# Kernel tuning notes

Measured on AMD Instinct MI355X. Metric: run time of the kernel, lower is better.

## Reference

```python
import jax, jax.numpy as jnp
import numpy as np

NUM_Q = 1000
DIM_S = 64
SIZE_M = 50
BATCH = 128
SEQ = 200


def setup_inputs() -> dict:
    key = jax.random.key(0)
    ks = jax.random.split(key, 16)
    s = 1.0 / np.sqrt(DIM_S)
    inp = {
        "q": jax.random.randint(ks[0], (BATCH, SEQ), 0, NUM_Q),
        "r": jax.random.randint(ks[1], (BATCH, SEQ), 0, 2),
        "at_s": jax.random.randint(ks[2], (BATCH, 16), 0, 30000),
        "at_m": jnp.ones((BATCH, 16), dtype=jnp.int64 if jax.config.jax_enable_x64 else jnp.int32),
        "k_emb": jax.random.normal(ks[3], (NUM_Q, DIM_S)) * s,
        "v_emb": jax.random.normal(ks[4], (2 * NUM_Q, DIM_S)) * s,
        "Mk": jax.random.normal(ks[5], (SIZE_M, DIM_S)) * s,
        "Mv0": jax.random.normal(ks[6], (SIZE_M, DIM_S)) * s,
        "We": jax.random.normal(ks[7], (DIM_S, DIM_S)) * s,
        "be": jnp.zeros((DIM_S,)),
        "Wa": jax.random.normal(ks[8], (DIM_S, DIM_S)) * s,
        "ba": jnp.zeros((DIM_S,)),
        "Wf": jax.random.normal(ks[9], (2 * DIM_S, DIM_S)) * s,
        "bf": jnp.zeros((DIM_S,)),
        "Wp": jax.random.normal(ks[10], (DIM_S, 1)) * s,
        "bp": jnp.zeros((1,)),
    }
    return inp


def reference(q, r, at_s, at_m, k_emb, v_emb, Mk, Mv0, We, be, Wa, ba, Wf, bf, Wp, bp):
    num_q = k_emb.shape[0]
    x = q + r * num_q                         # [B, n]
    k = k_emb[q]                              # [B, n, d]
    v = v_emb[x]                              # [B, n, d]
    w = jax.nn.softmax(jnp.einsum("bnd,md->bnm", k, Mk), axis=-1)  # [B, n, m]
    e = jax.nn.sigmoid(v @ We + be)           # erase gate [B, n, d]
    a = jnp.tanh(v @ Wa + ba)                 # add vector [B, n, d]

    B = q.shape[0]
    Mv_init = jnp.broadcast_to(Mv0[None], (B,) + Mv0.shape)  # [B, m, d]

    def step(Mvt, inp):
        et, at_, wt = inp                     # [B,d], [B,d], [B,m]
        Mvt = Mvt * (1.0 - wt[:, :, None] * et[:, None, :]) + wt[:, :, None] * at_[:, None, :]
        return Mvt, Mvt

    xs = (e.transpose(1, 0, 2), a.transpose(1, 0, 2), w.transpose(1, 0, 2))
    _, Mv_seq = jax.lax.scan(step, Mv_init, xs)             # [n, B, m, d]
    Mv = jnp.concatenate([Mv_init[None], Mv_seq], axis=0)   # [n+1, B, m, d]
    Mv = Mv.transpose(1, 0, 2, 3)                            # [B, n+1, m, d]

    read = jnp.einsum("bnm,bnmd->bnd", w, Mv[:, :-1])        # read from pre-update memory
    f = jnp.tanh(jnp.concatenate([read, k], axis=-1) @ Wf + bf)
    p = jax.nn.sigmoid((f @ Wp + bp)).squeeze(-1)            # [B, n]; dropout is identity at eval
    return p, Mv
```

## Files before the change

kernel.cpp:

```cpp
#include <hip/hip_runtime.h>
#include <hip/hip_bf16.h>

typedef __hip_bfloat16 bf16;

#define BATCH 128
#define SEQ   200
#define NUMQ  1000
#define DD    64
#define MM    50
#define MG    10
#define NMG   5
#define CHUNKS 10
#define CLEN   20


__device__ __forceinline__ float rdlane(float v, int j) {
    return __uint_as_float(__builtin_amdgcn_readlane(__float_as_uint(v), j));
}

__global__ __launch_bounds__(256) void k1_precompute(
    const int* __restrict__ q, const int* __restrict__ r,
    const float* __restrict__ k_emb, const float* __restrict__ v_emb,
    const float* __restrict__ Mk,
    const float* __restrict__ We, const float* __restrict__ be,
    const float* __restrict__ Wa, const float* __restrict__ ba,
    float* __restrict__ w_buf, float* __restrict__ e_buf, float* __restrict__ a_buf)
{
    __shared__ float Mk_l[MM][DD + 1];
    __shared__ float kv_l[4][128];

    const int tid = threadIdx.x;
    for (int i = tid; i < MM * DD; i += 256)
        Mk_l[i >> 6][i & 63] = Mk[i];

    const int w    = tid >> 6;
    const int lane = tid & 63;
    const int row  = blockIdx.x * 4 + w;

    int qi = q[row], ri = r[row];
    qi = min(max(qi, 0), NUMQ - 1);
    ri = min(max(ri, 0), 1);
    const int xi = qi + ri * NUMQ;

    kv_l[w][lane]      = k_emb[(size_t)qi * DD + lane];
    kv_l[w][64 + lane] = v_emb[(size_t)xi * DD + lane];
    __syncthreads();

    float s = 0.f;
    if (lane < MM) {
        #pragma unroll
        for (int dd = 0; dd < DD; ++dd)
            s += kv_l[w][dd] * Mk_l[lane][dd];
    }
    float mx = (lane < MM) ? s : -1e30f;
    #pragma unroll
    for (int off = 32; off >= 1; off >>= 1)
        mx = fmaxf(mx, __shfl_xor(mx, off, 64));
    float ex = (lane < MM) ? expf(s - mx) : 0.f;
    float sm = ex;
    #pragma unroll
    for (int off = 32; off >= 1; off >>= 1)
        sm += __shfl_xor(sm, off, 64);
    if (lane < MM)
        w_buf[(size_t)row * MM + lane] = ex / sm;

    float ea = be[lane], aa = ba[lane];
    #pragma unroll
    for (int dd = 0; dd < DD; ++dd) {
        const float vb = kv_l[w][64 + dd];
        ea = __builtin_fmaf(vb, We[dd * DD + lane], ea);
        aa = __builtin_fmaf(vb, Wa[dd * DD + lane], aa);
    }
    e_buf[(size_t)row * DD + lane] = 1.f / (1.f + expf(-ea));
    a_buf[(size_t)row * DD + lane] = tanhf(aa);
}

__global__ __launch_bounds__(640, 5) void k2_hier(
    const float* __restrict__ Mv0,
    const float* __restrict__ w_buf, const float* __restrict__ e_buf,
    const float* __restrict__ a_buf,
    float* __restrict__ read5_buf, float* __restrict__ out_Mv)
{
    __shared__ float S[MG][DD];

    const int blk  = blockIdx.x;
    const int b    = blk / NMG;
    const int mg   = blk % NMG;
    const int tid  = threadIdx.x;
    const int wv   = tid >> 6;
    const int lane = tid & 63;
    const int t0   = wv * CLEN;
    const int mb   = mg * MG;

    const float* wrow = w_buf + (size_t)b * SEQ * MM + mb;
    const float* erow = e_buf + (size_t)b * SEQ * DD;
    const float* arow = a_buf + (size_t)b * SEQ * DD;

    float A[MG], B[MG];
    #pragma unroll
    for (int j = 0; j < MG; ++j) { A[j] = 1.f; B[j] = 0.f; }

    float wreg = (lane < MG) ? wrow[(size_t)t0 * MM + lane] : 0.f;
    float e_n  = erow[(size_t)t0 * DD + lane];
    float a_n  = arow[(size_t)t0 * DD + lane];

    for (int tt = 0; tt < CLEN; ++tt) {
        const int t = t0 + tt;
        const float e_v = e_n, a_v = a_n, wcur = wreg;
        if (t + 1 < SEQ) {
            wreg = (lane < MG) ? wrow[(size_t)(t + 1) * MM + lane] : 0.f;
            e_n  = erow[(size_t)(t + 1) * DD + lane];
            a_n  = arow[(size_t)(t + 1) * DD + lane];
        }
        #pragma unroll
        for (int j = 0; j < MG; ++j) {
            const float wj = rdlane(wcur, j);
            const float f  = __builtin_fmaf(-wj, e_v, 1.f);
            A[j] *= f;
            B[j] = __builtin_fmaf(B[j], f, wj * a_v);
        }
    }

    float* outb = out_Mv + (size_t)b * (SEQ + 1) * MM * DD + (size_t)mb * DD;
    if (wv == 0) {
        #pragma unroll
        for (int j = 0; j < MG; ++j) {
            const float m0v = Mv0[(mb + j) * DD + lane];
            S[j][lane] = m0v;
            __builtin_nontemporal_store(m0v, &outb[j * DD + lane]);
        }
    }
    __syncthreads();

    float Mv[MG];
    for (int w = 0; w < CHUNKS; ++w) {
        if (wv == w) {
            #pragma unroll
            for (int j = 0; j < MG; ++j) {
                Mv[j] = S[j][lane];
                S[j][lane] = __builtin_fmaf(A[j], Mv[j], B[j]);
            }
        }
        __syncthreads();
    }

    float* rrow = read5_buf + ((size_t)mg * BATCH + b) * SEQ * DD;

    wreg = (lane < MG) ? wrow[(size_t)t0 * MM + lane] : 0.f;
    e_n  = erow[(size_t)t0 * DD + lane];
    a_n  = arow[(size_t)t0 * DD + lane];

    for (int tt = 0; tt < CLEN; ++tt) {
        const int t = t0 + tt;
        const float e_v = e_n, a_v = a_n, wcur = wreg;
        if (t + 1 < SEQ) {
            wreg = (lane < MG) ? wrow[(size_t)(t + 1) * MM + lane] : 0.f;
            e_n  = erow[(size_t)(t + 1) * DD + lane];
            a_n  = arow[(size_t)(t + 1) * DD + lane];
        }
        float* outt = outb + (size_t)(t + 1) * MM * DD;
        float racc0 = 0.f, racc1 = 0.f;
        #pragma unroll
        for (int j = 0; j < MG; ++j) {
            const float wj    = rdlane(wcur, j);
            const float m_old = Mv[j];
            if (j & 1) racc1 = __builtin_fmaf(wj, m_old, racc1);
            else       racc0 = __builtin_fmaf(wj, m_old, racc0);
            Mv[j] = __builtin_fmaf(wj, __builtin_fmaf(-e_v, m_old, a_v), m_old);
            __builtin_nontemporal_store(Mv[j], &outt[j * DD + lane]);
        }
        rrow[(size_t)t * DD + lane] = racc0 + racc1;
    }
}

__global__ __launch_bounds__(256) void k3_out(
    const int* __restrict__ q,
    const float* __restrict__ k_emb,
    const float* __restrict__ read5_buf,
    const float* __restrict__ Wf, const float* __restrict__ bfb,
    const float* __restrict__ Wp, const float* __restrict__ bp,
    float* __restrict__ out_p)
{
    __shared__ float rk[4][128];
    const int tid  = threadIdx.x;
    const int w    = tid >> 6;
    const int lane = tid & 63;
    const int row  = blockIdx.x * 4 + w;

    int qi = q[row];
    qi = min(max(qi, 0), NUMQ - 1);

    float rsum = 0.f;
    #pragma unroll
    for (int g = 0; g < NMG; ++g)
        rsum += read5_buf[((size_t)g * BATCH * SEQ + row) * DD + lane];
    rk[w][lane]      = rsum;
    rk[w][64 + lane] = k_emb[(size_t)qi * DD + lane];
    __syncthreads();

    float acc = bfb[lane];
    #pragma unroll
    for (int i = 0; i < 2 * DD; ++i)
        acc = __builtin_fmaf(rk[w][i], Wf[i * DD + lane], acc);
    const float f = tanhf(acc);

    float pv = f * Wp[lane];
    #pragma unroll
    for (int off = 32; off >= 1; off >>= 1)
        pv += __shfl_xor(pv, off, 64);

    if (lane == 0)
        out_p[row] = 1.f / (1.f + expf(-(pv + bp[0])));
}

__global__ __launch_bounds__(640) void dkvmn_fused(
    const int* q_, const int* r_,
    const float* k_emb, const float* v_emb, const float* Mk, const float* Mv0,
    const float* We, const float* be, const float* Wa, const float* ba,
    const float* Wf, const float* bfb, const float* Wp, const float* bp,
    float* out_p, float* out_Mv)
{
    __shared__ float Mk_l[MM][DD + 1];
    __shared__ bf16  ring[SEQ][DD];
    __shared__ int   q_row[SEQ], x_row[SEQ];
    __shared__ float kbuf[DD], vbuf[DD], vbuf2[DD];
    __shared__ float wst[MM], est[DD], ast[DD];
    __shared__ float partial[640];
    __shared__ float bias_e[DD], bias_a[DD];

    const int b    = blockIdx.x;
    const int tid  = threadIdx.x;
    const int wv   = tid >> 6;
    const int lane = tid & 63;

    for (int t = tid; t < SEQ; t += 640) {
        int qi = q_[b * SEQ + t], ri = r_[b * SEQ + t];
        qi = min(max(qi, 0), NUMQ - 1); ri = min(max(ri, 0), 1);
        q_row[t] = qi; x_row[t] = qi + ri * NUMQ;
    }
    for (int i = tid; i < MM * DD; i += 640) Mk_l[i >> 6][i & 63] = Mk[i];
    if (tid < DD) { bias_e[tid] = be[tid]; bias_a[tid] = ba[tid]; }

    const int d  = lane;
    const int m0 = wv * 5;
    float* outb = out_Mv + (size_t)b * (SEQ + 1) * MM * DD;
    float Mv[5];
    #pragma unroll
    for (int j = 0; j < 5; ++j) {
        Mv[j] = Mv0[(m0 + j) * DD + d];
        outb[(m0 + j) * DD + d] = Mv[j];
    }
    __syncthreads();

    float kf_n = 0.f, vf_n = 0.f, vf2_n = 0.f;
    if (wv == 0) kf_n  = k_emb[(size_t)q_row[0] * DD + lane];
    if (wv == 1) vf_n  = v_emb[(size_t)x_row[0] * DD + lane];
    if (wv == 2) vf2_n = v_emb[(size_t)x_row[0] * DD + lane];

    for (int t = 0; t < SEQ; ++t) {
        if (wv == 0) {
            kbuf[lane] = kf_n;
            if (t + 1 < SEQ) kf_n = k_emb[(size_t)q_row[t + 1] * DD + lane];
            float s = 0.f;
            if (lane < MM) {
                #pragma unroll
                for (int dd = 0; dd < DD; ++dd) s += kbuf[dd] * Mk_l[lane][dd];
            }
            float mx = (lane < MM) ? s : -1e30f;
            #pragma unroll
            for (int off = 32; off >= 1; off >>= 1) mx = fmaxf(mx, __shfl_xor(mx, off, 64));
            float ex = (lane < MM) ? expf(s - mx) : 0.f;
            float sm = ex;
            #pragma unroll
            for (int off = 32; off >= 1; off >>= 1) sm += __shfl_xor(sm, off, 64);
            if (lane < MM) wst[lane] = ex / sm;
        } else if (wv == 1) {
            vbuf[lane] = vf_n;
            if (t + 1 < SEQ) vf_n = v_emb[(size_t)x_row[t + 1] * DD + lane];
            float acc = bias_e[lane];
            #pragma unroll
            for (int dd = 0; dd < DD; ++dd) acc += vbuf[dd] * We[dd * DD + lane];
            est[lane] = 1.f / (1.f + expf(-acc));
        } else if (wv == 2) {
            vbuf2[lane] = vf2_n;
            if (t + 1 < SEQ) vf2_n = v_emb[(size_t)x_row[t + 1] * DD + lane];
            float acc = bias_a[lane];
            #pragma unroll
            for (int dd = 0; dd < DD; ++dd) acc += vbuf2[dd] * Wa[dd * DD + lane];
            ast[lane] = tanhf(acc);
        }
        __syncthreads();

        const float e_v = est[d];
        const float a_v = ast[d];
        float racc = 0.f;
        float* outt = outb + (size_t)(t + 1) * MM * DD;
        #pragma unroll
        for (int j = 0; j < 5; ++j) {
            const float wvv = wst[m0 + j];
            racc += wvv * Mv[j];
            Mv[j] = __builtin_fmaf(wvv, a_v - e_v * Mv[j], Mv[j]);
            outt[(m0 + j) * DD + d] = Mv[j];
        }
        partial[tid] = racc;
        __syncthreads();

        if (tid < DD) {
            float rr = 0.f;
            #pragma unroll
            for (int g = 0; g < 10; ++g) rr += partial[g * 64 + tid];
            ring[t][tid] = (bf16)rr;
        }
    }
    __syncthreads();

    for (int t = wv; t < SEQ; t += 10) {
        const int qi = q_row[t];
        const float kreg = k_emb[(size_t)qi * DD + lane];
        float acc = bfb[lane];
        #pragma unroll
        for (int i = 0; i < DD; ++i) acc += (float)ring[t][i] * Wf[i * DD + lane];
        #pragma unroll
        for (int i = 0; i < DD; ++i) acc += __shfl(kreg, i, 64) * Wf[(DD + i) * DD + lane];
        const float f = tanhf(acc);
        float pv = f * Wp[lane];
        #pragma unroll
        for (int off = 32; off >= 1; off >>= 1) pv += __shfl_xor(pv, off, 64);
        if (lane == 0)
            out_p[(size_t)b * SEQ + t] = 1.f / (1.f + expf(-(pv + bp[0])));
    }
}

extern "C" void kernel_launch(void* const* d_in, const int* in_sizes, int n_in,
                              void* d_out, int out_size, void* d_ws, size_t ws_size,
                              hipStream_t stream) {
    const int*   q     = (const int*)  d_in[0];
    const int*   r     = (const int*)  d_in[1];
    const float* k_emb = (const float*)d_in[4];
    const float* v_emb = (const float*)d_in[5];
    const float* Mk    = (const float*)d_in[6];
    const float* Mv0   = (const float*)d_in[7];
    const float* We    = (const float*)d_in[8];
    const float* be    = (const float*)d_in[9];
    const float* Wa    = (const float*)d_in[10];
    const float* ba    = (const float*)d_in[11];
    const float* Wf    = (const float*)d_in[12];
    const float* bfb   = (const float*)d_in[13];
    const float* Wp    = (const float*)d_in[14];
    const float* bp    = (const float*)d_in[15];

    float* out_p  = (float*)d_out;
    float* out_Mv = (float*)d_out + BATCH * SEQ;

    const size_t N_W  = (size_t)BATCH * SEQ * MM;
    const size_t N_D  = (size_t)BATCH * SEQ * DD;
    const size_t WS_NEEDED = (N_W + (2 + NMG) * N_D) * sizeof(float);

    const int rows = BATCH * SEQ;

    if (ws_size >= WS_NEEDED) {
        float* w_buf     = (float*)d_ws;
        float* e_buf     = w_buf + N_W;
        float* a_buf     = e_buf + N_D;
        float* read5_buf = a_buf + N_D;

        hipLaunchKernelGGL(k1_precompute, dim3(rows / 4), dim3(256), 0, stream,
                           q, r, k_emb, v_emb, Mk, We, be, Wa, ba, w_buf, e_buf, a_buf);
        hipLaunchKernelGGL(k2_hier, dim3(BATCH * NMG), dim3(640), 0, stream,
                           Mv0, w_buf, e_buf, a_buf, read5_buf, out_Mv);
        hipLaunchKernelGGL(k3_out, dim3(rows / 4), dim3(256), 0, stream,
                           q, k_emb, read5_buf, Wf, bfb, Wp, bp, out_p);
    } else {
        hipLaunchKernelGGL(dkvmn_fused, dim3(BATCH), dim3(640), 0, stream,
                           q, r, k_emb, v_emb, Mk, Mv0, We, be, Wa, ba,
                           Wf, bfb, Wp, bp, out_p, out_Mv);
    }
}
```

Baseline: 159.9 us.

## Split scan into checkpoint-state kernel and parallel replay kernel fused with output head

The hierarchical scan kernel now only computes memory checkpoints at 20 positions per batch and writes them to a small states buffer. A new replay kernel launches one block per batch and chunk, rebuilds the 10 steps of each chunk from its checkpoint, and writes the full Mv history. The same kernel also performs the read reduction and the output MLP, so the read5 buffer and the separate k3 kernel go away. This spreads the dominant Mv write traffic over many more blocks. The cost is some recomputation of the recurrence and the extra checkpoint writes and reads. The nontemporal stores are also changed to plain stores.

```diff
diff --git a/kernel.cpp b/kernel.cpp
--- a/kernel.cpp
+++ b/kernel.cpp
@@ -12,6 +12,8 @@
 #define NMG   5
 #define CHUNKS 10
 #define CLEN   20
+#define CR     20
+#define CRL    10
 
 
 __device__ __forceinline__ float rdlane(float v, int j) {
@@ -75,11 +77,11 @@
     a_buf[(size_t)row * DD + lane] = tanhf(aa);
 }
 
-__global__ __launch_bounds__(640, 5) void k2_hier(
+__global__ __launch_bounds__(640, 4) void k2s_states(
     const float* __restrict__ Mv0,
     const float* __restrict__ w_buf, const float* __restrict__ e_buf,
     const float* __restrict__ a_buf,
-    float* __restrict__ read5_buf, float* __restrict__ out_Mv)
+    float* __restrict__ states)
 {
     __shared__ float S[MG][DD];
 
@@ -121,14 +123,10 @@
         }
     }
 
-    float* outb = out_Mv + (size_t)b * (SEQ + 1) * MM * DD + (size_t)mb * DD;
     if (wv == 0) {
         #pragma unroll
-        for (int j = 0; j < MG; ++j) {
-            const float m0v = Mv0[(mb + j) * DD + lane];
-            S[j][lane] = m0v;
-            __builtin_nontemporal_store(m0v, &outb[j * DD + lane]);
-        }
+        for (int j = 0; j < MG; ++j)
+            S[j][lane] = Mv0[(mb + j) * DD + lane];
     }
     __syncthreads();
 
@@ -144,13 +142,15 @@
         __syncthreads();
     }
 
-    float* rrow = read5_buf + ((size_t)mg * BATCH + b) * SEQ * DD;
+    float* st0 = states + (((size_t)(b * NMG + mg)) * CR + 2 * wv) * (MG * DD);
+    #pragma unroll
+    for (int j = 0; j < MG; ++j)
+        st0[j * DD + lane] = Mv[j];
 
     wreg = (lane < MG) ? wrow[(size_t)t0 * MM + lane] : 0.f;
     e_n  = erow[(size_t)t0 * DD + lane];
     a_n  = arow[(size_t)t0 * DD + lane];
-
-    for (int tt = 0; tt < CLEN; ++tt) {
+    for (int tt = 0; tt < CRL; ++tt) {
         const int t = t0 + tt;
         const float e_v = e_n, a_v = a_n, wcur = wreg;
         if (t + 1 < SEQ) {
@@ -158,6 +158,68 @@
             e_n  = erow[(size_t)(t + 1) * DD + lane];
             a_n  = arow[(size_t)(t + 1) * DD + lane];
         }
+        #pragma unroll
+        for (int j = 0; j < MG; ++j) {
+            const float wj = rdlane(wcur, j);
+            Mv[j] = __builtin_fmaf(wj, __builtin_fmaf(-e_v, Mv[j], a_v), Mv[j]);
+        }
+    }
+    float* st1 = states + (((size_t)(b * NMG + mg)) * CR + 2 * wv + 1) * (MG * DD);
+    #pragma unroll
+    for (int j = 0; j < MG; ++j)
+        st1[j * DD + lane] = Mv[j];
+}
+
+__global__ __launch_bounds__(320, 6) void k2r_replay(
+    const int* __restrict__ q,
+    const float* __restrict__ k_emb,
+    const float* __restrict__ w_buf, const float* __restrict__ e_buf,
+    const float* __restrict__ a_buf,
+    const float* __restrict__ states,
+    const float* __restrict__ Wf, const float* __restrict__ bfb,
+    const float* __restrict__ Wp, const float* __restrict__ bp,
+    float* __restrict__ out_p, float* __restrict__ out_Mv)
+{
+    __shared__ float rpart[NMG][CRL][DD];
+
+    const int blk  = blockIdx.x;
+    const int b    = blk / CR;
+    const int c    = blk % CR;
+    const int tid  = threadIdx.x;
+    const int mg   = tid >> 6;
+    const int lane = tid & 63;
+    const int t0   = c * CRL;
+    const int mb   = mg * MG;
+
+    const float* st = states + (((size_t)(b * NMG + mg)) * CR + c) * (MG * DD);
+    float Mv[MG];
+    #pragma unroll
+    for (int j = 0; j < MG; ++j)
+        Mv[j] = st[j * DD + lane];
+
+    float* outb = out_Mv + (size_t)b * (SEQ + 1) * MM * DD + (size_t)mb * DD;
+    if (c == 0) {
+        #pragma unroll
+        for (int j = 0; j < MG; ++j)
+            outb[j * DD + lane] = Mv[j];
+    }
+
+    const float* wrow = w_buf + (size_t)b * SEQ * MM + mb;
+    const float* erow = e_buf + (size_t)b * SEQ * DD;
+    const float* arow = a_buf + (size_t)b * SEQ * DD;
+
+    float wreg = (lane < MG) ? wrow[(size_t)t0 * MM + lane] : 0.f;
+    float e_n  = erow[(size_t)t0 * DD + lane];
+    float a_n  = arow[(size_t)t0 * DD + lane];
+
+    for (int tt = 0; tt < CRL; ++tt) {
+        const int t = t0 + tt;
+        const float e_v = e_n, a_v = a_n, wcur = wreg;
+        if (t + 1 < SEQ) {
+            wreg = (lane < MG) ? wrow[(size_t)(t + 1) * MM + lane] : 0.f;
+            e_n  = erow[(size_t)(t + 1) * DD + lane];
+            a_n  = arow[(size_t)(t + 1) * DD + lane];
+        }
         float* outt = outb + (size_t)(t + 1) * MM * DD;
         float racc0 = 0.f, racc1 = 0.f;
         #pragma unroll
@@ -167,50 +229,43 @@
             if (j & 1) racc1 = __builtin_fmaf(wj, m_old, racc1);
             else       racc0 = __builtin_fmaf(wj, m_old, racc0);
             Mv[j] = __builtin_fmaf(wj, __builtin_fmaf(-e_v, m_old, a_v), m_old);
-            __builtin_nontemporal_store(Mv[j], &outt[j * DD + lane]);
-        }
-        rrow[(size_t)t * DD + lane] = racc0 + racc1;
-    }
-}
-
-__global__ __launch_bounds__(256) void k3_out(
-    const int* __restrict__ q,
-    const float* __restrict__ k_emb,
-    const float* __restrict__ read5_buf,
-    const float* __restrict__ Wf, const float* __restrict__ bfb,
-    const float* __restrict__ Wp, const float* __restrict__ bp,
-    float* __restrict__ out_p)
-{
-    __shared__ float rk[4][128];
-    const int tid  = threadIdx.x;
-    const int w    = tid >> 6;
-    const int lane = tid & 63;
-    const int row  = blockIdx.x * 4 + w;
-
-    int qi = q[row];
-    qi = min(max(qi, 0), NUMQ - 1);
-
-    float rsum = 0.f;
-    #pragma unroll
-    for (int g = 0; g < NMG; ++g)
-        rsum += read5_buf[((size_t)g * BATCH * SEQ + row) * DD + lane];
-    rk[w][lane]      = rsum;
-    rk[w][64 + lane] = k_emb[(size_t)qi * DD + lane];
+            outt[j * DD + lane] = Mv[j];
+        }
+        rpart[mg][tt][lane] = racc0 + racc1;
+    }
     __syncthreads();
 
-    float acc = bfb[lane];
-    #pragma unroll
-    for (int i = 0; i < 2 * DD; ++i)
-        acc = __builtin_fmaf(rk[w][i], Wf[i * DD + lane], acc);
-    const float f = tanhf(acc);
-
-    float pv = f * Wp[lane];
-    #pragma unroll
-    for (int off = 32; off >= 1; off >>= 1)
-        pv += __shfl_xor(pv, off, 64);
-
-    if (lane == 0)
-        out_p[row] = 1.f / (1.f + expf(-(pv + bp[0])));
+    const float bf_l = bfb[lane];
+    const float wp_l = Wp[lane];
+    #pragma unroll
+    for (int s = 0; s < 2; ++s) {
+        const int tt = mg * 2 + s;
+        const int t  = t0 + tt;
+        float rsum = rpart[0][tt][lane];
+        #pragma unroll
+        for (int g = 1; g < NMG; ++g)
+            rsum += rpart[g][tt][lane];
+
+        int qi = q[b * SEQ + t];
+        qi = min(max(qi, 0), NUMQ - 1);
+        const float kreg = k_emb[(size_t)qi * DD + lane];
+
+        float acc = bf_l;
+        #pragma unroll
+        for (int i = 0; i < DD; ++i)
+            acc = __builtin_fmaf(__shfl(rsum, i, 64), Wf[i * DD + lane], acc);
+        #pragma unroll
+        for (int i = 0; i < DD; ++i)
+            acc = __builtin_fmaf(__shfl(kreg, i, 64), Wf[(DD + i) * DD + lane], acc);
+        const float f = tanhf(acc);
+
+        float pv = f * wp_l;
+        #pragma unroll
+        for (int off = 32; off >= 1; off >>= 1)
+            pv += __shfl_xor(pv, off, 64);
+        if (lane == 0)
+            out_p[(size_t)b * SEQ + t] = 1.f / (1.f + expf(-(pv + bp[0])));
+    }
 }
 
 __global__ __launch_bounds__(640) void dkvmn_fused(
@@ -354,22 +409,24 @@
 
     const size_t N_W  = (size_t)BATCH * SEQ * MM;
     const size_t N_D  = (size_t)BATCH * SEQ * DD;
-    const size_t WS_NEEDED = (N_W + (2 + NMG) * N_D) * sizeof(float);
+    const size_t N_ST = (size_t)BATCH * NMG * CR * MG * DD;
+    const size_t WS_NEEDED = (N_W + 2 * N_D + N_ST) * sizeof(float);
 
     const int rows = BATCH * SEQ;
 
     if (ws_size >= WS_NEEDED) {
-        float* w_buf     = (float*)d_ws;
-        float* e_buf     = w_buf + N_W;
-        float* a_buf     = e_buf + N_D;
-        float* read5_buf = a_buf + N_D;
+        float* w_buf  = (float*)d_ws;
+        float* e_buf  = w_buf + N_W;
+        float* a_buf  = e_buf + N_D;
+        float* states = a_buf + N_D;
 
         hipLaunchKernelGGL(k1_precompute, dim3(rows / 4), dim3(256), 0, stream,
                            q, r, k_emb, v_emb, Mk, We, be, Wa, ba, w_buf, e_buf, a_buf);
-        hipLaunchKernelGGL(k2_hier, dim3(BATCH * NMG), dim3(640), 0, stream,
-                           Mv0, w_buf, e_buf, a_buf, read5_buf, out_Mv);
-        hipLaunchKernelGGL(k3_out, dim3(rows / 4), dim3(256), 0, stream,
-                           q, k_emb, read5_buf, Wf, bfb, Wp, bp, out_p);
+        hipLaunchKernelGGL(k2s_states, dim3(BATCH * NMG), dim3(640), 0, stream,
+                           Mv0, w_buf, e_buf, a_buf, states);
+        hipLaunchKernelGGL(k2r_replay, dim3(BATCH * CR), dim3(320), 0, stream,
+                           q, k_emb, w_buf, e_buf, a_buf, states,
+                           Wf, bfb, Wp, bp, out_p, out_Mv);
     } else {
         hipLaunchKernelGGL(dkvmn_fused, dim3(BATCH), dim3(640), 0, stream,
                            q, r, k_emb, v_emb, Mk, Mv0, We, be, Wa, ba,
```

Result: slower. 530.0 us (+231.5%).
